# Kernel tuning notes

Hardware: AMD Instinct MI355X
Metric: run time of the kernel (lower is better)

## Reference

```python
import jax, jax.numpy as jnp
import numpy as np

N, C, SUBVEC, K, DOUT, DEPTH = 16384, 64, 16, 16, 1024, 4


def setup_inputs() -> dict:
    key = jax.random.key(0)
    k1, k2, k3, k4, k5 = jax.random.split(key, 5)
    x = jax.random.normal(k1, (N, C * SUBVEC), dtype=jnp.float32)
    split_idxs = jax.random.randint(k2, (C, DEPTH), 0, SUBVEC, dtype=jnp.int32)
    split_vals = jax.random.normal(k3, (C, DEPTH, K // 2), dtype=jnp.float32)
    lookup_tables = jax.random.normal(k4, (C, K, DOUT), dtype=jnp.float32)
    bias = jax.random.normal(k5, (DOUT,), dtype=jnp.float32)
    return {"x": x, "split_idxs": split_idxs, "split_vals": split_vals,
            "lookup_tables": lookup_tables, "bias": bias}


def _encode(x_sub, split_idxs, split_vals):
    # x_sub: (n, C, subvec_len); split_idxs: (C, 4); split_vals: (C, 4, 8)
    n = x_sub.shape[0]
    c_idx = jnp.arange(C)
    enc = jnp.zeros((n, C), dtype=jnp.int32)
    for t in range(DEPTH):  # fixed tree depth 4
        xv = x_sub[:, c_idx, split_idxs[:, t]]            # (n, C) selected feature per codebook
        thresh = split_vals[c_idx[None, :], t, enc]       # (n, C) per-node threshold
        enc = 2 * enc + (xv > thresh).astype(jnp.int32)
    return enc  # values in [0, 16)


def reference(x, split_idxs, split_vals, lookup_tables, bias):
    n = x.shape[0]
    x_sub = x.reshape(n, C, SUBVEC)
    enc = _encode(x_sub, split_idxs, split_vals)           # (n, C) int32
    onehot = jax.nn.one_hot(enc, K, dtype=x.dtype)         # (n, C, K)
    out = jnp.einsum('nck,cko->no', onehot, lookup_tables) # sum over codebooks of LUT rows
    return out + bias
```

## Files before the change

kernel.cpp:

```cpp
#include <hip/hip_runtime.h>

#define NN    16384
#define CBN   64
#define SUBV  16
#define KCODE 16
#define DOUTN 1024
#define DEP   4

typedef short bf16x8 __attribute__((ext_vector_type(8)));
typedef float f32x16 __attribute__((ext_vector_type(16)));

static __device__ __forceinline__ unsigned short f2bf(float f) {
  unsigned int u = __float_as_uint(f);
  u += 0x7FFFu + ((u >> 16) & 1u);
  return (unsigned short)(u >> 16);
}

static __device__ __forceinline__ void gld16(const void* g, void* l) {
  __builtin_amdgcn_global_load_lds(
      (const __attribute__((address_space(1))) unsigned int*)g,
      (__attribute__((address_space(3))) unsigned int*)(uintptr_t)l, 16, 0, 0);
}

__global__ __launch_bounds__(256) void prep_k(
    const float* __restrict__ x, const int* __restrict__ split_idxs,
    const float* __restrict__ split_vals, const float* __restrict__ Tg,
    unsigned char* __restrict__ codes, unsigned int* __restrict__ Tswz) {
  const int t = threadIdx.x;

  if (blockIdx.x < 64) {
    const int img = blockIdx.x;
    const int g = img >> 3, ch = img & 7;
    unsigned int* dst = Tswz + (size_t)img * 8192;
    const int colq = t & 31, kp = (t >> 5) & 7;
    #pragma unroll
    for (int cl = 0; cl < 8; ++cl) {
      const float* g0 = Tg + ((size_t)((ch * 8 + cl) * KCODE + 2 * kp)) * DOUTN
                        + g * 128 + colq * 4;
      float4 r0 = *(const float4*)g0;
      float4 r1 = *(const float4*)(g0 + DOUTN);
      unsigned int pk[4] = {
        f2bf(r0.x) | ((unsigned int)f2bf(r1.x) << 16),
        f2bf(r0.y) | ((unsigned int)f2bf(r1.y) << 16),
        f2bf(r0.z) | ((unsigned int)f2bf(r1.z) << 16),
        f2bf(r0.w) | ((unsigned int)f2bf(r1.w) << 16)};
      unsigned key = (unsigned)(colq & 7) << 2;
      #pragma unroll
      for (int j = 0; j < 4; ++j)
        dst[cl * 1024 + ((((unsigned)(colq * 4 + j)) * 8 + (unsigned)kp) ^ key)]
            = pk[j];
    }
    return;
  }

  __shared__ __align__(16) float xs[8][SUBV * CBN];
  __shared__ int   sidxT[DEP * CBN];
  __shared__ float svalT[DEP * (KCODE / 2) * CBN];
  if (t < DEP * CBN) {
    int d = t >> 6, c = t & 63;
    sidxT[t] = split_idxs[c * DEP + d];
  }
  for (int i = t; i < DEP * (KCODE / 2) * CBN; i += 256) {
    int c = i & 63, de = i >> 6, d = de >> 3, e = de & 7;
    svalT[i] = split_vals[(c * DEP + d) * (KCODE / 2) + e];
  }
  const int n0 = (blockIdx.x - 64) * 8;
  const float4* xg = (const float4*)(x + (size_t)n0 * DOUTN);
  #pragma unroll
  for (int i = 0; i < 8; ++i) {
    int li = t + i * 256;
    int r = li >> 8, cpos = li & 255;
    float4 v = xg[r * 256 + cpos];
    int c = cpos >> 2, q = cpos & 3;
    *(float4*)&xs[r][c * SUBV + ((q ^ (c & 3)) << 2)] = v;
  }
  __syncthreads();
  const int c = t & 63, rg = t >> 6;
  #pragma unroll
  for (int i = 0; i < 2; ++i) {
    int nl = rg * 2 + i;
    int e = 0;
    #pragma unroll
    for (int d = 0; d < DEP; ++d) {
      int si = sidxT[d * 64 + c];
      float xv = xs[nl][c * SUBV + (((si >> 2) ^ (c & 3)) << 2) + (si & 3)];
      float th = svalT[(d * 8 + e) * 64 + c];
      e = 2 * e + (xv > th ? 1 : 0);
    }
    codes[(size_t)(n0 + nl) * CBN + c] = (unsigned char)e;
  }
}

__global__ __launch_bounds__(1024, 4) void maddness_mfma(
    const unsigned int* __restrict__ Tswz, const float* __restrict__ bias,
    const unsigned char* __restrict__ codes, float* __restrict__ out) {
  __shared__ __align__(16) unsigned int Tb[32768];

  const int t = threadIdx.x;
  const int wid = t >> 6, lane = t & 63, lrow = lane & 31, h = lane >> 5;
  const int g16 = blockIdx.x, g8 = g16 >> 1, half = g16 & 1;
  const int n0 = blockIdx.y * 1024;
  const char* img = (const char*)Tswz + (size_t)g8 * 8 * 32768;

  #pragma unroll
  for (int i = 0; i < 8; ++i) {
    int gs = wid * 8 + i;
    int ch = gs >> 4, s16 = gs & 15, cl = s16 >> 1, pc = s16 & 1;
    gld16(img + ch * 32768 + cl * 4096 + half * 2048 + pc * 1024 + lane * 16,
          (char*)Tb + gs * 1024);
  }

  f32x16 acc[2][2];
  #pragma unroll
  for (int rt = 0; rt < 2; ++rt)
    #pragma unroll
    for (int ct = 0; ct < 2; ++ct)
      #pragma unroll
      for (int e = 0; e < 16; ++e) acc[rt][ct][e] = 0.f;

  const unsigned char* crow = codes + (size_t)(n0 + wid * 64 + lrow) * CBN;
  unsigned long long qwA[2], qwB[2];
  qwA[0] = *(const unsigned long long*)(crow);
  qwA[1] = *(const unsigned long long*)(crow + 32 * CBN);

  __syncthreads();

  #pragma unroll
  for (int ch = 0; ch < 8; ++ch) {
    if (ch < 7) {
      qwB[0] = *(const unsigned long long*)(crow + (ch + 1) * 8);
      qwB[1] = *(const unsigned long long*)(crow + 32 * CBN + (ch + 1) * 8);
    }
    const unsigned short* tb = (const unsigned short*)Tb + ch * 8192;
    __builtin_amdgcn_s_setprio(1);
    #pragma unroll
    for (int cl = 0; cl < 8; ++cl) {
      bf16x8 bv[2];
      #pragma unroll
      for (int ct = 0; ct < 2; ++ct) {
        unsigned col_loc = (unsigned)(ct * 32 + lrow);
        unsigned uidx = (unsigned)(cl * 1024)
                      + ((col_loc * 16 + (unsigned)h * 8)
                         ^ (((col_loc >> 2) & 7u) << 3));
        bv[ct] = *(const bf16x8*)(tb + uidx);
      }
      #pragma unroll
      for (int rt = 0; rt < 2; ++rt) {
        int c = (int)((qwA[rt] >> (8 * cl)) & 255);
        int p = c >> 1;
        unsigned s = 0x3F80u << ((c & 1) << 4);
        union { unsigned int u[4]; bf16x8 v; } A;
        #pragma unroll
        for (int j = 0; j < 4; ++j) A.u[j] = (p == h * 4 + j) ? s : 0u;
        acc[rt][0] = __builtin_amdgcn_mfma_f32_32x32x16_bf16(A.v, bv[0], acc[rt][0], 0, 0, 0);
        acc[rt][1] = __builtin_amdgcn_mfma_f32_32x32x16_bf16(A.v, bv[1], acc[rt][1], 0, 0, 0);
      }
    }
    __builtin_amdgcn_s_setprio(0);
    qwA[0] = qwB[0]; qwA[1] = qwB[1];
  }

  #pragma unroll
  for (int ct = 0; ct < 2; ++ct) {
    const int col = g16 * 64 + ct * 32 + lrow;
    const float bval = bias[col];
    #pragma unroll
    for (int rt = 0; rt < 2; ++rt)
      #pragma unroll
      for (int r = 0; r < 16; ++r) {
        int row = n0 + wid * 64 + rt * 32 + (r & 3) + 8 * (r >> 2) + 4 * h;
        out[(size_t)row * DOUTN + col] = acc[rt][ct][r] + bval;
      }
  }
}

extern "C" void kernel_launch(void* const* d_in, const int* in_sizes, int n_in,
                              void* d_out, int out_size, void* d_ws, size_t ws_size,
                              hipStream_t stream) {
  const float* x    = (const float*)d_in[0];
  const int*   sidx = (const int*)d_in[1];
  const float* sval = (const float*)d_in[2];
  const float* Tg   = (const float*)d_in[3];
  const float* bias = (const float*)d_in[4];
  float* out = (float*)d_out;
  unsigned char* codes = (unsigned char*)d_ws;
  unsigned int*  Tswz  = (unsigned int*)((char*)d_ws + (1 << 20));

  prep_k<<<64 + NN / 8, 256, 0, stream>>>(x, sidx, sval, Tg, codes, Tswz);
  maddness_mfma<<<dim3(16, 16), 1024, 0, stream>>>(Tswz, bias, codes, out);
}
```

Baseline: 52.82 us.

## Fuse encode and LUT-MFMA stages into one cooperative kernel with grid sync

Merges the prep kernel and the MFMA kernel into a single cooperative launch of 256 blocks. Each block converts and swizzles its own LUT column slice to bf16 directly into shared memory, encodes 64 rows of codes, then waits on a grid-wide barrier before running the MFMA accumulation. This removes the intermediate swizzled LUT buffer, its global round trip and a second kernel launch. In exchange each block re-reads and re-converts the LUT redundantly, the x loads are strided rather than staged through shared memory, and the grid sync adds latency. It also staggers codebook order per wave and drops setprio.

New measurement: 93.33 us. 1.77x slower.

```diff
diff --git a/kernel.cpp b/kernel.cpp
--- a/kernel.cpp
+++ b/kernel.cpp
@@ -1,4 +1,7 @@
 #include <hip/hip_runtime.h>
+#include <hip/hip_cooperative_groups.h>
+
+namespace cg = cooperative_groups;
 
 #define NN    16384
 #define CBN   64
@@ -16,99 +19,68 @@
   return (unsigned short)(u >> 16);
 }
 
-static __device__ __forceinline__ void gld16(const void* g, void* l) {
-  __builtin_amdgcn_global_load_lds(
-      (const __attribute__((address_space(1))) unsigned int*)g,
-      (__attribute__((address_space(3))) unsigned int*)(uintptr_t)l, 16, 0, 0);
-}
-
-__global__ __launch_bounds__(256) void prep_k(
+__global__ __launch_bounds__(1024, 4) void fused_k(
     const float* __restrict__ x, const int* __restrict__ split_idxs,
     const float* __restrict__ split_vals, const float* __restrict__ Tg,
-    unsigned char* __restrict__ codes, unsigned int* __restrict__ Tswz) {
-  const int t = threadIdx.x;
-
-  if (blockIdx.x < 64) {
-    const int img = blockIdx.x;
-    const int g = img >> 3, ch = img & 7;
-    unsigned int* dst = Tswz + (size_t)img * 8192;
-    const int colq = t & 31, kp = (t >> 5) & 7;
-    #pragma unroll
-    for (int cl = 0; cl < 8; ++cl) {
-      const float* g0 = Tg + ((size_t)((ch * 8 + cl) * KCODE + 2 * kp)) * DOUTN
-                        + g * 128 + colq * 4;
-      float4 r0 = *(const float4*)g0;
-      float4 r1 = *(const float4*)(g0 + DOUTN);
-      unsigned int pk[4] = {
-        f2bf(r0.x) | ((unsigned int)f2bf(r1.x) << 16),
-        f2bf(r0.y) | ((unsigned int)f2bf(r1.y) << 16),
-        f2bf(r0.z) | ((unsigned int)f2bf(r1.z) << 16),
-        f2bf(r0.w) | ((unsigned int)f2bf(r1.w) << 16)};
-      unsigned key = (unsigned)(colq & 7) << 2;
-      #pragma unroll
-      for (int j = 0; j < 4; ++j)
-        dst[cl * 1024 + ((((unsigned)(colq * 4 + j)) * 8 + (unsigned)kp) ^ key)]
-            = pk[j];
-    }
-    return;
-  }
-
-  __shared__ __align__(16) float xs[8][SUBV * CBN];
+    const float* __restrict__ bias, unsigned char* __restrict__ codes,
+    float* __restrict__ out) {
+  __shared__ __align__(16) unsigned int Tb[32768];
   __shared__ int   sidxT[DEP * CBN];
   __shared__ float svalT[DEP * (KCODE / 2) * CBN];
+
+  const int t = threadIdx.x;
+  const int b = blockIdx.x;
+  const int cg16 = b & 15, rg16 = b >> 4;
+
   if (t < DEP * CBN) {
     int d = t >> 6, c = t & 63;
     sidxT[t] = split_idxs[c * DEP + d];
   }
-  for (int i = t; i < DEP * (KCODE / 2) * CBN; i += 256) {
+  for (int i = t; i < DEP * (KCODE / 2) * CBN; i += 1024) {
     int c = i & 63, de = i >> 6, d = de >> 3, e = de & 7;
     svalT[i] = split_vals[(c * DEP + d) * (KCODE / 2) + e];
   }
-  const int n0 = (blockIdx.x - 64) * 8;
-  const float4* xg = (const float4*)(x + (size_t)n0 * DOUTN);
-  #pragma unroll
-  for (int i = 0; i < 8; ++i) {
-    int li = t + i * 256;
-    int r = li >> 8, cpos = li & 255;
-    float4 v = xg[r * 256 + cpos];
-    int c = cpos >> 2, q = cpos & 3;
-    *(float4*)&xs[r][c * SUBV + ((q ^ (c & 3)) << 2)] = v;
+
+  {
+    const int col = t & 63;
+    #pragma unroll
+    for (int cb0 = 0; cb0 < 4; ++cb0) {
+      const int cb = cb0 * 16 + (t >> 6);
+      const float* src = Tg + (size_t)cb * KCODE * DOUTN + cg16 * 64 + col;
+      float v[16];
+      #pragma unroll
+      for (int k = 0; k < 16; ++k) v[k] = src[k * DOUTN];
+      unsigned int* dst = Tb + (cb >> 3) * 4096 + (cb & 7) * 512;
+      const unsigned key = (((unsigned)col >> 2) & 7u) << 2;
+      #pragma unroll
+      for (int kp = 0; kp < 8; ++kp) {
+        unsigned int pk = f2bf(v[2 * kp]) | ((unsigned int)f2bf(v[2 * kp + 1]) << 16);
+        dst[((unsigned)(col * 8 + kp)) ^ key] = pk;
+      }
+    }
   }
   __syncthreads();
-  const int c = t & 63, rg = t >> 6;
-  #pragma unroll
-  for (int i = 0; i < 2; ++i) {
-    int nl = rg * 2 + i;
-    int e = 0;
+
+  {
+    const int c = t & 63, rg = t >> 6;
+    const float* xr = x + (size_t)(b * 64 + rg * 4) * DOUTN + c * SUBV;
     #pragma unroll
-    for (int d = 0; d < DEP; ++d) {
-      int si = sidxT[d * 64 + c];
-      float xv = xs[nl][c * SUBV + (((si >> 2) ^ (c & 3)) << 2) + (si & 3)];
-      float th = svalT[(d * 8 + e) * 64 + c];
-      e = 2 * e + (xv > th ? 1 : 0);
+    for (int i = 0; i < 4; ++i) {
+      int e = 0;
+      #pragma unroll
+      for (int d = 0; d < DEP; ++d) {
+        float xv = xr[i * DOUTN + sidxT[d * 64 + c]];
+        float th = svalT[(d * 8 + e) * 64 + c];
+        e = 2 * e + (xv > th ? 1 : 0);
+      }
+      codes[(size_t)(b * 64 + rg * 4 + i) * CBN + c] = (unsigned char)e;
     }
-    codes[(size_t)(n0 + nl) * CBN + c] = (unsigned char)e;
   }
-}
 
-__global__ __launch_bounds__(1024, 4) void maddness_mfma(
-    const unsigned int* __restrict__ Tswz, const float* __restrict__ bias,
-    const unsigned char* __restrict__ codes, float* __restrict__ out) {
-  __shared__ __align__(16) unsigned int Tb[32768];
+  cg::this_grid().sync();
 
-  const int t = threadIdx.x;
   const int wid = t >> 6, lane = t & 63, lrow = lane & 31, h = lane >> 5;
-  const int g16 = blockIdx.x, g8 = g16 >> 1, half = g16 & 1;
-  const int n0 = blockIdx.y * 1024;
-  const char* img = (const char*)Tswz + (size_t)g8 * 8 * 32768;
-
-  #pragma unroll
-  for (int i = 0; i < 8; ++i) {
-    int gs = wid * 8 + i;
-    int ch = gs >> 4, s16 = gs & 15, cl = s16 >> 1, pc = s16 & 1;
-    gld16(img + ch * 32768 + cl * 4096 + half * 2048 + pc * 1024 + lane * 16,
-          (char*)Tb + gs * 1024);
-  }
+  const int n0 = rg16 * 1024;
 
   f32x16 acc[2][2];
   #pragma unroll
@@ -120,19 +92,21 @@
 
   const unsigned char* crow = codes + (size_t)(n0 + wid * 64 + lrow) * CBN;
   unsigned long long qwA[2], qwB[2];
-  qwA[0] = *(const unsigned long long*)(crow);
-  qwA[1] = *(const unsigned long long*)(crow + 32 * CBN);
-
-  __syncthreads();
+  {
+    const int ch0 = wid & 7;
+    qwA[0] = *(const unsigned long long*)(crow + ch0 * 8);
+    qwA[1] = *(const unsigned long long*)(crow + 32 * CBN + ch0 * 8);
+  }
 
   #pragma unroll
-  for (int ch = 0; ch < 8; ++ch) {
-    if (ch < 7) {
-      qwB[0] = *(const unsigned long long*)(crow + (ch + 1) * 8);
-      qwB[1] = *(const unsigned long long*)(crow + 32 * CBN + (ch + 1) * 8);
+  for (int i = 0; i < 8; ++i) {
+    const int ch = (wid + i) & 7;
+    if (i < 7) {
+      const int chn = (wid + i + 1) & 7;
+      qwB[0] = *(const unsigned long long*)(crow + chn * 8);
+      qwB[1] = *(const unsigned long long*)(crow + 32 * CBN + chn * 8);
     }
     const unsigned short* tb = (const unsigned short*)Tb + ch * 8192;
-    __builtin_amdgcn_s_setprio(1);
     #pragma unroll
     for (int cl = 0; cl < 8; ++cl) {
       bf16x8 bv[2];
@@ -156,13 +130,12 @@
         acc[rt][1] = __builtin_amdgcn_mfma_f32_32x32x16_bf16(A.v, bv[1], acc[rt][1], 0, 0, 0);
       }
     }
-    __builtin_amdgcn_s_setprio(0);
     qwA[0] = qwB[0]; qwA[1] = qwB[1];
   }
 
   #pragma unroll
   for (int ct = 0; ct < 2; ++ct) {
-    const int col = g16 * 64 + ct * 32 + lrow;
+    const int col = cg16 * 64 + ct * 32 + lrow;
     const float bval = bias[col];
     #pragma unroll
     for (int rt = 0; rt < 2; ++rt)
@@ -184,8 +157,9 @@
   const float* bias = (const float*)d_in[4];
   float* out = (float*)d_out;
   unsigned char* codes = (unsigned char*)d_ws;
-  unsigned int*  Tswz  = (unsigned int*)((char*)d_ws + (1 << 20));
 
-  prep_k<<<64 + NN / 8, 256, 0, stream>>>(x, sidx, sval, Tg, codes, Tswz);
-  maddness_mfma<<<dim3(16, 16), 1024, 0, stream>>>(Tswz, bias, codes, out);
+  void* args[] = {(void*)&x, (void*)&sidx, (void*)&sval, (void*)&Tg,
+                  (void*)&bias, (void*)&codes, (void*)&out};
+  hipLaunchCooperativeKernel((const void*)fused_k, dim3(256), dim3(1024),
+                             args, 0, stream);
 }
```

## Restructure MFMA loop per column tile with staggered chunk order and batched LDS loads

Applied to the files above, without the earlier changes.

Reorders the main loop so each wave processes one column tile at a time across all chunks. Each wave starts at a different chunk offset (wid-based), which spreads LDS bank accesses across waves. B fragments for four codebooks are loaded in a batch ahead of their MFMAs to hide LDS latency, and the setprio hints are removed. Code bytes are now reloaded from global memory twice (once per column tile) and the software prefetch of codes is dropped, so load latency may be exposed more.

Result: no change. 52.51 us (-0.6%).

```diff
diff --git a/kernel.cpp b/kernel.cpp
--- a/kernel.cpp
+++ b/kernel.cpp
@@ -118,46 +118,55 @@
       #pragma unroll
       for (int e = 0; e < 16; ++e) acc[rt][ct][e] = 0.f;
 
-  const unsigned char* crow = codes + (size_t)(n0 + wid * 64 + lrow) * CBN;
-  unsigned long long qwA[2], qwB[2];
-  qwA[0] = *(const unsigned long long*)(crow);
-  qwA[1] = *(const unsigned long long*)(crow + 32 * CBN);
+  const unsigned char* crow0 = codes + (size_t)(n0 + wid * 64 + lrow) * CBN;
+  const unsigned char* crow1 = crow0 + 32 * CBN;
 
   __syncthreads();
 
   #pragma unroll
-  for (int ch = 0; ch < 8; ++ch) {
-    if (ch < 7) {
-      qwB[0] = *(const unsigned long long*)(crow + (ch + 1) * 8);
-      qwB[1] = *(const unsigned long long*)(crow + 32 * CBN + (ch + 1) * 8);
-    }
-    const unsigned short* tb = (const unsigned short*)Tb + ch * 8192;
-    __builtin_amdgcn_s_setprio(1);
-    #pragma unroll
-    for (int cl = 0; cl < 8; ++cl) {
-      bf16x8 bv[2];
-      #pragma unroll
-      for (int ct = 0; ct < 2; ++ct) {
-        unsigned col_loc = (unsigned)(ct * 32 + lrow);
-        unsigned uidx = (unsigned)(cl * 1024)
-                      + ((col_loc * 16 + (unsigned)h * 8)
-                         ^ (((col_loc >> 2) & 7u) << 3));
-        bv[ct] = *(const bf16x8*)(tb + uidx);
-      }
-      #pragma unroll
-      for (int rt = 0; rt < 2; ++rt) {
-        int c = (int)((qwA[rt] >> (8 * cl)) & 255);
-        int p = c >> 1;
-        unsigned s = 0x3F80u << ((c & 1) << 4);
-        union { unsigned int u[4]; bf16x8 v; } A;
+  for (int ct = 0; ct < 2; ++ct) {
+    const unsigned col_loc = (unsigned)(ct * 32 + lrow);
+    const unsigned rb = (col_loc * 16 + (unsigned)h * 8)
+                      ^ (((col_loc >> 2) & 7u) << 3);
+    const unsigned short* tb0 = (const unsigned short*)Tb + rb;
+
+    #pragma unroll
+    for (int i = 0; i < 8; ++i) {
+      const int ch = (wid + i) & 7;
+      const unsigned long long qw0 = *(const unsigned long long*)(crow0 + ch * 8);
+      const unsigned long long qw1 = *(const unsigned long long*)(crow1 + ch * 8);
+      const unsigned short* tbc = tb0 + ch * 8192;
+
+      bf16x8 bva[4], bvb[4];
+      #pragma unroll
+      for (int k = 0; k < 4; ++k)
+        bva[k] = *(const bf16x8*)(tbc + k * 1024);
+
+      #pragma unroll
+      for (int hb = 0; hb < 2; ++hb) {
+        if (hb == 0) {
+          #pragma unroll
+          for (int k = 0; k < 4; ++k)
+            bvb[k] = *(const bf16x8*)(tbc + (4 + k) * 1024);
+        }
         #pragma unroll
-        for (int j = 0; j < 4; ++j) A.u[j] = (p == h * 4 + j) ? s : 0u;
-        acc[rt][0] = __builtin_amdgcn_mfma_f32_32x32x16_bf16(A.v, bv[0], acc[rt][0], 0, 0, 0);
-        acc[rt][1] = __builtin_amdgcn_mfma_f32_32x32x16_bf16(A.v, bv[1], acc[rt][1], 0, 0, 0);
+        for (int k = 0; k < 4; ++k) {
+          const int cl = hb * 4 + k;
+          const bf16x8 bv = hb ? bvb[k] : bva[k];
+          #pragma unroll
+          for (int rt = 0; rt < 2; ++rt) {
+            const unsigned long long q = rt ? qw1 : qw0;
+            int c = (int)((q >> (8 * cl)) & 255);
+            int p = c >> 1;
+            unsigned s = 0x3F80u << ((c & 1) << 4);
+            union { unsigned int u[4]; bf16x8 v; } A;
+            #pragma unroll
+            for (int j = 0; j < 4; ++j) A.u[j] = (p == h * 4 + j) ? s : 0u;
+            acc[rt][ct] = __builtin_amdgcn_mfma_f32_32x32x16_bf16(A.v, bv, acc[rt][ct], 0, 0, 0);
+          }
+        }
       }
     }
-    __builtin_amdgcn_s_setprio(0);
-    qwA[0] = qwB[0]; qwA[1] = qwB[1];
   }
 
   #pragma unroll
```

## Fuse encoding and MFMA LUT accumulation into one cooperative kernel with grid sync

Applied to the files above, without the earlier changes.

The LUT bf16 conversion moves into its own small kernel, and the per-row encoding merges into the MFMA kernel, which is launched cooperatively with 256 blocks. Each block encodes 64 rows by gathering the selected x features straight from global memory, then does a grid-wide sync before reading codes for its 1024-row tile. The LUT load into LDS overlaps with the encoding phase. Codebook chunk order is rotated per wave, and the code prefetch and setprio are removed. This saves a kernel launch and a separate pass but adds a grid barrier and scattered 4-byte gathers from x.

After: 105.1 us. +99.0%, slower.

```diff
diff --git a/kernel.cpp b/kernel.cpp
--- a/kernel.cpp
+++ b/kernel.cpp
@@ -1,4 +1,7 @@
 #include <hip/hip_runtime.h>
+#include <hip/hip_cooperative_groups.h>
+
+namespace cg = cooperative_groups;
 
 #define NN    16384
 #define CBN   64
@@ -22,93 +25,95 @@
       (__attribute__((address_space(3))) unsigned int*)(uintptr_t)l, 16, 0, 0);
 }
 
-__global__ __launch_bounds__(256) void prep_k(
+__global__ __launch_bounds__(256) void convert_k(
+    const float* __restrict__ Tg, unsigned int* __restrict__ Tswz) {
+  const int t = threadIdx.x;
+  const int img = blockIdx.x;
+  const int g = img >> 3, ch = img & 7;
+  unsigned int* dst = Tswz + (size_t)img * 8192;
+  const int colq = t & 31, kp = (t >> 5) & 7;
+  #pragma unroll
+  for (int cl = 0; cl < 8; ++cl) {
+    const float* g0 = Tg + ((size_t)((ch * 8 + cl) * KCODE + 2 * kp)) * DOUTN
+                      + g * 128 + colq * 4;
+    float4 r0 = *(const float4*)g0;
+    float4 r1 = *(const float4*)(g0 + DOUTN);
+    unsigned int pk[4] = {
+      f2bf(r0.x) | ((unsigned int)f2bf(r1.x) << 16),
+      f2bf(r0.y) | ((unsigned int)f2bf(r1.y) << 16),
+      f2bf(r0.z) | ((unsigned int)f2bf(r1.z) << 16),
+      f2bf(r0.w) | ((unsigned int)f2bf(r1.w) << 16)};
+    unsigned key = (unsigned)(colq & 7) << 2;
+    #pragma unroll
+    for (int j = 0; j < 4; ++j)
+      dst[cl * 1024 + ((((unsigned)(colq * 4 + j)) * 8 + (unsigned)kp) ^ key)]
+          = pk[j];
+  }
+}
+
+__global__ __launch_bounds__(1024, 4) void fused_k(
     const float* __restrict__ x, const int* __restrict__ split_idxs,
-    const float* __restrict__ split_vals, const float* __restrict__ Tg,
-    unsigned char* __restrict__ codes, unsigned int* __restrict__ Tswz) {
+    const float* __restrict__ split_vals, const unsigned int* __restrict__ Tswz,
+    const float* __restrict__ bias, unsigned char* __restrict__ codes,
+    float* __restrict__ out) {
+  __shared__ __align__(16) unsigned int Tb[32768];
+  __shared__ int   sidxT[DEP * CBN];
+  __shared__ float svalT[DEP * (KCODE / 2) * CBN];
+
   const int t = threadIdx.x;
+  const int b = blockIdx.x;
+  const int g16 = b & 15;
+  const int n0 = (b >> 4) * 1024;
+  const int wid = t >> 6, lane = t & 63, lrow = lane & 31, h = lane >> 5;
 
-  if (blockIdx.x < 64) {
-    const int img = blockIdx.x;
-    const int g = img >> 3, ch = img & 7;
-    unsigned int* dst = Tswz + (size_t)img * 8192;
-    const int colq = t & 31, kp = (t >> 5) & 7;
+  {
+    const int g8 = g16 >> 1, half = g16 & 1;
+    const char* img = (const char*)Tswz + (size_t)g8 * 8 * 32768;
     #pragma unroll
-    for (int cl = 0; cl < 8; ++cl) {
-      const float* g0 = Tg + ((size_t)((ch * 8 + cl) * KCODE + 2 * kp)) * DOUTN
-                        + g * 128 + colq * 4;
-      float4 r0 = *(const float4*)g0;
-      float4 r1 = *(const float4*)(g0 + DOUTN);
-      unsigned int pk[4] = {
-        f2bf(r0.x) | ((unsigned int)f2bf(r1.x) << 16),
-        f2bf(r0.y) | ((unsigned int)f2bf(r1.y) << 16),
-        f2bf(r0.z) | ((unsigned int)f2bf(r1.z) << 16),
-        f2bf(r0.w) | ((unsigned int)f2bf(r1.w) << 16)};
-      unsigned key = (unsigned)(colq & 7) << 2;
-      #pragma unroll
-      for (int j = 0; j < 4; ++j)
-        dst[cl * 1024 + ((((unsigned)(colq * 4 + j)) * 8 + (unsigned)kp) ^ key)]
-            = pk[j];
+    for (int i = 0; i < 8; ++i) {
+      int gs = wid * 8 + i;
+      int ch = gs >> 4, s16 = gs & 15, cl = s16 >> 1, pc = s16 & 1;
+      gld16(img + ch * 32768 + cl * 4096 + half * 2048 + pc * 1024 + lane * 16,
+            (char*)Tb + gs * 1024);
     }
-    return;
   }
 
-  __shared__ __align__(16) float xs[8][SUBV * CBN];
-  __shared__ int   sidxT[DEP * CBN];
-  __shared__ float svalT[DEP * (KCODE / 2) * CBN];
   if (t < DEP * CBN) {
     int d = t >> 6, c = t & 63;
     sidxT[t] = split_idxs[c * DEP + d];
   }
-  for (int i = t; i < DEP * (KCODE / 2) * CBN; i += 256) {
+  for (int i = t; i < DEP * (KCODE / 2) * CBN; i += 1024) {
     int c = i & 63, de = i >> 6, d = de >> 3, e = de & 7;
     svalT[i] = split_vals[(c * DEP + d) * (KCODE / 2) + e];
   }
-  const int n0 = (blockIdx.x - 64) * 8;
-  const float4* xg = (const float4*)(x + (size_t)n0 * DOUTN);
-  #pragma unroll
-  for (int i = 0; i < 8; ++i) {
-    int li = t + i * 256;
-    int r = li >> 8, cpos = li & 255;
-    float4 v = xg[r * 256 + cpos];
-    int c = cpos >> 2, q = cpos & 3;
-    *(float4*)&xs[r][c * SUBV + ((q ^ (c & 3)) << 2)] = v;
+  __syncthreads();
+
+  {
+    const int c = lane;
+    const size_t r0 = (size_t)b * 64 + wid * 4;
+    const float* xr = x + r0 * DOUTN + c * SUBV;
+    const int si0 = sidxT[c], si1 = sidxT[64 + c],
+              si2 = sidxT[128 + c], si3 = sidxT[192 + c];
+    float xv[4][4];
+    #pragma unroll
+    for (int i = 0; i < 4; ++i) {
+      const float* xri = xr + (size_t)i * DOUTN;
+      xv[i][0] = xri[si0]; xv[i][1] = xri[si1];
+      xv[i][2] = xri[si2]; xv[i][3] = xri[si3];
+    }
+    #pragma unroll
+    for (int i = 0; i < 4; ++i) {
+      int e = 0;
+      #pragma unroll
+      for (int d = 0; d < DEP; ++d) {
+        float th = svalT[(d * 8 + e) * 64 + c];
+        e = 2 * e + (xv[i][d] > th ? 1 : 0);
+      }
+      codes[(r0 + i) * CBN + c] = (unsigned char)e;
+    }
   }
-  __syncthreads();
-  const int c = t & 63, rg = t >> 6;
-  #pragma unroll
-  for (int i = 0; i < 2; ++i) {
-    int nl = rg * 2 + i;
-    int e = 0;
-    #pragma unroll
-    for (int d = 0; d < DEP; ++d) {
-      int si = sidxT[d * 64 + c];
-      float xv = xs[nl][c * SUBV + (((si >> 2) ^ (c & 3)) << 2) + (si & 3)];
-      float th = svalT[(d * 8 + e) * 64 + c];
-      e = 2 * e + (xv > th ? 1 : 0);
-    }
-    codes[(size_t)(n0 + nl) * CBN + c] = (unsigned char)e;
-  }
-}
 
-__global__ __launch_bounds__(1024, 4) void maddness_mfma(
-    const unsigned int* __restrict__ Tswz, const float* __restrict__ bias,
-    const unsigned char* __restrict__ codes, float* __restrict__ out) {
-  __shared__ __align__(16) unsigned int Tb[32768];
-
-  const int t = threadIdx.x;
-  const int wid = t >> 6, lane = t & 63, lrow = lane & 31, h = lane >> 5;
-  const int g16 = blockIdx.x, g8 = g16 >> 1, half = g16 & 1;
-  const int n0 = blockIdx.y * 1024;
-  const char* img = (const char*)Tswz + (size_t)g8 * 8 * 32768;
-
-  #pragma unroll
-  for (int i = 0; i < 8; ++i) {
-    int gs = wid * 8 + i;
-    int ch = gs >> 4, s16 = gs & 15, cl = s16 >> 1, pc = s16 & 1;
-    gld16(img + ch * 32768 + cl * 4096 + half * 2048 + pc * 1024 + lane * 16,
-          (char*)Tb + gs * 1024);
-  }
+  cg::this_grid().sync();
 
   f32x16 acc[2][2];
   #pragma unroll
@@ -118,21 +123,15 @@
       #pragma unroll
       for (int e = 0; e < 16; ++e) acc[rt][ct][e] = 0.f;
 
-  const unsigned char* crow = codes + (size_t)(n0 + wid * 64 + lrow) * CBN;
-  unsigned long long qwA[2], qwB[2];
-  qwA[0] = *(const unsigned long long*)(crow);
-  qwA[1] = *(const unsigned long long*)(crow + 32 * CBN);
-
-  __syncthreads();
+  const unsigned char* crow0 = codes + (size_t)(n0 + wid * 64 + lrow) * CBN;
+  const unsigned char* crow1 = crow0 + 32 * CBN;
 
   #pragma unroll
-  for (int ch = 0; ch < 8; ++ch) {
-    if (ch < 7) {
-      qwB[0] = *(const unsigned long long*)(crow + (ch + 1) * 8);
-      qwB[1] = *(const unsigned long long*)(crow + 32 * CBN + (ch + 1) * 8);
-    }
-    const unsigned short* tb = (const unsigned short*)Tb + ch * 8192;
-    __builtin_amdgcn_s_setprio(1);
+  for (int i = 0; i < 8; ++i) {
+    const int ch = (wid + i) & 7;
+    const unsigned long long qw0 = *(const unsigned long long*)(crow0 + ch * 8);
+    const unsigned long long qw1 = *(const unsigned long long*)(crow1 + ch * 8);
+    const unsigned short* tbc = (const unsigned short*)Tb + ch * 8192;
     #pragma unroll
     for (int cl = 0; cl < 8; ++cl) {
       bf16x8 bv[2];
@@ -142,11 +141,11 @@
         unsigned uidx = (unsigned)(cl * 1024)
                       + ((col_loc * 16 + (unsigned)h * 8)
                          ^ (((col_loc >> 2) & 7u) << 3));
-        bv[ct] = *(const bf16x8*)(tb + uidx);
+        bv[ct] = *(const bf16x8*)(tbc + uidx);
       }
       #pragma unroll
       for (int rt = 0; rt < 2; ++rt) {
-        int c = (int)((qwA[rt] >> (8 * cl)) & 255);
+        int c = (int)(((rt ? qw1 : qw0) >> (8 * cl)) & 255);
         int p = c >> 1;
         unsigned s = 0x3F80u << ((c & 1) << 4);
         union { unsigned int u[4]; bf16x8 v; } A;
@@ -156,8 +155,6 @@
         acc[rt][1] = __builtin_amdgcn_mfma_f32_32x32x16_bf16(A.v, bv[1], acc[rt][1], 0, 0, 0);
       }
     }
-    __builtin_amdgcn_s_setprio(0);
-    qwA[0] = qwB[0]; qwA[1] = qwB[1];
   }
 
   #pragma unroll
@@ -186,6 +183,10 @@
   unsigned char* codes = (unsigned char*)d_ws;
   unsigned int*  Tswz  = (unsigned int*)((char*)d_ws + (1 << 20));
 
-  prep_k<<<64 + NN / 8, 256, 0, stream>>>(x, sidx, sval, Tg, codes, Tswz);
-  maddness_mfma<<<dim3(16, 16), 1024, 0, stream>>>(Tswz, bias, codes, out);
+  convert_k<<<64, 256, 0, stream>>>(Tg, Tswz);
+  const unsigned int* TswzC = Tswz;
+  void* args[] = {(void*)&x, (void*)&sidx, (void*)&sval, (void*)&TswzC,
+                  (void*)&bias, (void*)&codes, (void*)&out};
+  hipLaunchCooperativeKernel((const void*)fused_k, dim3(256), dim3(1024),
+                             args, 0, stream);
 }
```
